# Kernel optimization log

Hardware: AMD Instinct MI355X
Metric: run time of the kernel (lower is better)

The kernel has to match this reference:

```python
import jax, jax.numpy as jnp
import numpy as np

N_CELLS, C_N, K, D_N = 128, 256, 16, 64
G, HS, HM, HMOD, HEADS = 8, 128, 128, 64, 4


def setup_inputs() -> dict:
    key = jax.random.key(0)
    ks = list(jax.random.split(key, 12))
    rng = np.random.default_rng(0)
    # top-K neighbors per neuron within each cell, self excluded, sorted (as in __init__)
    scores = rng.random((N_CELLS, C_N, C_N), dtype=np.float32)
    scores[:, np.arange(C_N), np.arange(C_N)] = -np.inf
    topk = np.argpartition(-scores, K, axis=-1)[..., :K]
    conn_idx = jnp.asarray(np.sort(topk, axis=-1).astype(np.int32))
    cell_to_group = jnp.asarray((np.arange(N_CELLS) % G).astype(np.int32))

    def nrm(k, shape, scale):
        return jax.random.normal(k, shape, dtype=jnp.float32) * scale

    inp = {
        'h': nrm(ks[0], (N_CELLS, C_N, D_N), 1.0),
        'neuron_id': nrm(ks[1], (N_CELLS, C_N, D_N), 0.02),
        'neuron_key': nrm(ks[2], (N_CELLS, C_N, D_N), 0.02),
        'state_w1': nrm(ks[3], (HS, 2 * D_N), (2.0 / (2 * D_N)) ** 0.5),
        'state_b1': jnp.zeros((HS,), jnp.float32),
        'state_gs1': jnp.ones((G, HS), jnp.float32),
        'state_gb1': jnp.zeros((G, HS), jnp.float32),
        'state_w2': nrm(ks[4], (D_N, HS), 0.1 * (2.0 / HS) ** 0.5),
        'state_b2': jnp.zeros((D_N,), jnp.float32),
        'state_gs2': jnp.ones((G, D_N), jnp.float32),
        'state_gb2': jnp.zeros((G, D_N), jnp.float32),
        'msg_w1': nrm(ks[5], (HM, 2 * D_N), (2.0 / (2 * D_N)) ** 0.5),
        'msg_b1': jnp.zeros((HM,), jnp.float32),
        'msg_gs1': jnp.ones((G, HM), jnp.float32),
        'msg_gb1': jnp.zeros((G, HM), jnp.float32),
        'msg_w2': nrm(ks[6], (D_N, HM), 0.1 * (2.0 / HM) ** 0.5),
        'msg_b2': jnp.zeros((D_N,), jnp.float32),
        'msg_gs2': jnp.ones((G, D_N), jnp.float32),
        'msg_gb2': jnp.zeros((G, D_N), jnp.float32),
        'mod_w1': nrm(ks[7], (N_CELLS, D_N, HMOD), (2.0 / D_N) ** 0.5),
        'mod_b1': jnp.zeros((N_CELLS, HMOD), jnp.float32),
        'mod_w2': nrm(ks[8], (N_CELLS, HMOD, D_N), 0.01 * (2.0 / HMOD) ** 0.5),
        'mod_b2': jnp.zeros((N_CELLS, D_N), jnp.float32),
        'conn_idx': conn_idx,
        'cell_to_group': cell_to_group,
    }
    return inp


def reference(h, neuron_id, neuron_key,
              state_w1, state_b1, state_gs1, state_gb1,
              state_w2, state_b2, state_gs2, state_gb2,
              msg_w1, msg_b1, msg_gs1, msg_gb1,
              msg_w2, msg_b2, msg_gs2, msg_gb2,
              mod_w1, mod_b1, mod_w2, mod_b2,
              conn_idx, cell_to_group):
    g = cell_to_group  # [N]
    dh = D_N // HEADS
    gather = jax.vmap(lambda per_cell, idx: per_cell[idx])  # [C,D],[C,K] -> [C,K,D]

    nbr = gather(h, conn_idx)          # [N,C,K,D] neighbor states
    kid = gather(neuron_id, conn_idx)  # [N,C,K,D] neighbor identity vectors

    # multi-head attention weights over the K neighbors
    q = neuron_key.reshape(N_CELLS, C_N, HEADS, dh)
    kk = kid.reshape(N_CELLS, C_N, K, HEADS, dh)
    logits = jnp.einsum('nchd,nckhd->nckh', q, kk) / (dh ** 0.5)
    attn = jax.nn.softmax(logits, axis=2)  # softmax over K

    # per-edge message MLP with per-group gain/bias
    x = jnp.concatenate([nbr, jnp.broadcast_to(h[:, :, None, :], nbr.shape)], axis=-1)  # [N,C,K,2D]
    m1 = jax.nn.gelu(jnp.einsum('nckf,hf->nckh', x, msg_w1) + msg_b1)
    m1 = m1 * msg_gs1[g][:, None, None, :] + msg_gb1[g][:, None, None, :]
    m2 = jnp.einsum('nckh,dh->nckd', m1, msg_w2) + msg_b2
    m2 = m2 * msg_gs2[g][:, None, None, :] + msg_gb2[g][:, None, None, :]

    # attention-weighted aggregation over neighbors
    m2h = m2.reshape(N_CELLS, C_N, K, HEADS, dh)
    agg = jnp.einsum('nckh,nckhd->nchd', attn, m2h).reshape(N_CELLS, C_N, D_N)

    # state-update MLP with per-group gain/bias
    s_in = jnp.concatenate([h, agg], axis=-1)  # [N,C,2D]
    s1 = jax.nn.gelu(jnp.einsum('ncf,hf->nch', s_in, state_w1) + state_b1)
    s1 = s1 * state_gs1[g][:, None, :] + state_gb1[g][:, None, :]
    delta = jnp.einsum('nch,dh->ncd', s1, state_w2) + state_b2
    delta = delta * state_gs2[g][:, None, :] + state_gb2[g][:, None, :]

    # per-cell batched modulation MLP (mod_w1/mod_w2) gating the update
    pooled = h.mean(axis=1)  # [N,D]
    mh = jnp.tanh(jnp.einsum('nd,ndh->nh', pooled, mod_w1) + mod_b1)
    gate = jnp.tanh(jnp.einsum('nh,nho->no', mh, mod_w2) + mod_b2)  # [N,D]

    return h + gate[:, None, :] * delta
```

## Files before the change

kernel.cpp:

```cpp
#include <hip/hip_runtime.h>
#include <hip/hip_bf16.h>

#define N_CELLS 128
#define C_N     256
#define K_NB    16
#define D_N     64
#define G_N     8
#define HS      128
#define HM      128
#define HMOD    64

typedef __bf16 bf16x8 __attribute__((ext_vector_type(8)));
typedef float  f32x4v __attribute__((ext_vector_type(4)));
typedef _Float16 half2_t __attribute__((ext_vector_type(2)));


__device__ __forceinline__ unsigned cvtpk(float lo, float hi) {
    __hip_bfloat162 t = __float22bfloat162_rn(float2{lo, hi});
    return *reinterpret_cast<unsigned*>(&t);
}

__device__ __forceinline__ unsigned short f2bf(float f) {
    return (unsigned short)(cvtpk(f, 0.f) & 0xffffu);
}

__device__ __forceinline__ float bflo(unsigned u) { return __uint_as_float(u << 16); }
__device__ __forceinline__ float bfhi(unsigned u) { return __uint_as_float(u & 0xffff0000u); }

__device__ __forceinline__ half2_t pkrtz(float lo, float hi) {
    return __builtin_bit_cast(half2_t, __builtin_amdgcn_cvt_pkrtz(lo, hi));
}

__device__ __forceinline__ half2_t h2(unsigned u) {
    return __builtin_bit_cast(half2_t, u);
}

__device__ __forceinline__ f32x4v mfma16(uint4 a, uint4 b, f32x4v c) {
    return __builtin_amdgcn_mfma_f32_16x16x32_bf16(
        __builtin_bit_cast(bf16x8, a), __builtin_bit_cast(bf16x8, b), c, 0, 0, 0);
}

__device__ __forceinline__ float gelu_f(float x) {
    float x2 = x * x;
    float u  = x * fmaf(x2, 0.044715f, 1.0f);
    float e  = __expf(1.5957691216057308f * u);
    float r  = __builtin_amdgcn_rcpf(e + 1.0f);
    return x - x * r;
}

__device__ __forceinline__ float sgelu(float x) {
    float e = __expf(-1.702f * x);
    float r = __builtin_amdgcn_rcpf(e + 1.0f);
    return x * r;
}

__device__ __forceinline__ float tanh_fast(float z) {
    float e = __expf(2.0f * z);
    return 1.0f - 2.0f / (e + 1.0f);
}

__device__ __forceinline__ uint4 packf8(const float* p) {
    float4 a = *(const float4*)p, b = *(const float4*)(p + 4);
    return make_uint4(cvtpk(a.x, a.y), cvtpk(a.z, a.w), cvtpk(b.x, b.y), cvtpk(b.z, b.w));
}

__device__ __forceinline__ void load_w2_folded(
    const float* __restrict__ w2, const float* __restrict__ gs1,
    const float* __restrict__ gb1, const float* __restrict__ gs2,
    const float* __restrict__ b2, const float* __restrict__ gb2,
    int g, int lrow, int lgrp, uint4 wf[4][4], float c2[4])
{
    #pragma unroll
    for (int nb2 = 0; nb2 < 4; ++nb2) {
        int d = nb2 * 16 + lrow;
        float gs2d = gs2[g * 64 + d];
        float cgb = 0.0f;
        #pragma unroll
        for (int kf = 0; kf < 4; ++kf) {
            int k0 = kf * 32 + lgrp * 8;
            const float* wp = w2 + d * 128 + k0;
            float4 wa = *(const float4*)wp, wb = *(const float4*)(wp + 4);
            const float* gp = gs1 + g * 128 + k0;
            float4 ga = *(const float4*)gp, gbv = *(const float4*)(gp + 4);
            const float* bp = gb1 + g * 128 + k0;
            float4 ba = *(const float4*)bp, bbv = *(const float4*)(bp + 4);
            cgb += wa.x*ba.x + wa.y*ba.y + wa.z*ba.z + wa.w*ba.w
                 + wb.x*bbv.x + wb.y*bbv.y + wb.z*bbv.z + wb.w*bbv.w;
            wf[nb2][kf] = make_uint4(
                cvtpk(wa.x*ga.x*gs2d,  wa.y*ga.y*gs2d),
                cvtpk(wa.z*ga.z*gs2d,  wa.w*ga.w*gs2d),
                cvtpk(wb.x*gbv.x*gs2d, wb.y*gbv.y*gs2d),
                cvtpk(wb.z*gbv.z*gs2d, wb.w*gbv.w*gs2d));
        }
        cgb += __shfl_xor(cgb, 16);
        cgb += __shfl_xor(cgb, 32);
        c2[nb2] = fmaf(gs2d, cgb + b2[d], gb2[g * 64 + d]);
    }
}


__global__ __launch_bounds__(1024) void gate_kernel(
    const float* __restrict__ h,
    const float* __restrict__ mod_w1, const float* __restrict__ mod_b1,
    const float* __restrict__ mod_w2, const float* __restrict__ mod_b2,
    float* __restrict__ gatep)
{
    __shared__ float red[16][64];
    __shared__ float pooled[64];
    __shared__ float mh[64];
    int n = blockIdx.x, tid = threadIdx.x;
    int d = tid & 63, part = tid >> 6;
    const float* hn = h + (size_t)n * C_N * 64;
    float acc = 0.0f;
    #pragma unroll 4
    for (int i = 0; i < 16; ++i) acc += hn[(part * 16 + i) * 64 + d];
    red[part][d] = acc;
    __syncthreads();
    if (tid < 64) {
        float s = 0.0f;
        #pragma unroll
        for (int p = 0; p < 16; ++p) s += red[p][d];
        pooled[d] = s * (1.0f / 256.0f);
    }
    __syncthreads();
    if (tid < 64) {
        float a1 = mod_b1[n * HMOD + d];
        for (int q = 0; q < 64; ++q)
            a1 = fmaf(pooled[q], mod_w1[((size_t)n * 64 + q) * HMOD + d], a1);
        mh[d] = tanh_fast(a1);
    }
    __syncthreads();
    if (tid < 64) {
        float a2 = mod_b2[n * 64 + d];
        for (int q = 0; q < HMOD; ++q)
            a2 = fmaf(mh[q], mod_w2[((size_t)n * HMOD + q) * 64 + d], a2);
        gatep[n * 64 + d] = tanh_fast(a2);
    }
}


__global__ __launch_bounds__(512, 4) void node_kernel(
    const float* __restrict__ h, const float* __restrict__ msg_w1,
    const float* __restrict__ msg_b1,
    unsigned short* __restrict__ yws, unsigned short* __restrict__ bews)
{
    __shared__ __align__(16) unsigned short ybuf_all[8][16 * 256];
    int tid = threadIdx.x, bid = blockIdx.x;
    int n = bid >> 1;
    int wave = tid >> 6, lane = tid & 63;
    int lrow = lane & 15, lgrp = lane >> 4;
    int c0 = (bid & 1) * 128 + wave * 16;
    unsigned short* ybuf = ybuf_all[wave];

    uint4 bf[2];
    {
        const float* hp = h + ((size_t)n * C_N + (c0 + lrow)) * 64;
        bf[0] = packf8(hp + lgrp * 8);
        bf[1] = packf8(hp + 32 + lgrp * 8);
    }
    for (int nbM = 0; nbM < 16; ++nbM) {
        int o = nbM * 16 + lrow;
        uint4 af[2];
        #pragma unroll
        for (int kf = 0; kf < 2; ++kf) {
            int k = kf * 32 + lgrp * 8;
            const float* wp = (o < 128) ? (msg_w1 + (size_t)o * 128 + k)
                                        : (msg_w1 + (size_t)(o - 128) * 128 + 64 + k);
            af[kf] = packf8(wp);
        }
        f32x4v acc = {0.f, 0.f, 0.f, 0.f};
        acc = mfma16(af[0], bf[0], acc);
        acc = mfma16(af[1], bf[1], acc);
        float4 addv = {0.f, 0.f, 0.f, 0.f};
        if (nbM >= 8) addv = *(const float4*)(msg_b1 + (nbM - 8) * 16 + lgrp * 4);
        uint2 pk = make_uint2(cvtpk(acc[0] + addv.x, acc[1] + addv.y),
                              cvtpk(acc[2] + addv.z, acc[3] + addv.w));
        int byte = lrow * 512 + ((nbM * 32 + lgrp * 8) ^ ((lrow & 7) << 4));
        *reinterpret_cast<uint2*>(reinterpret_cast<char*>(ybuf) + byte) = pk;
    }
    #pragma unroll
    for (int pass = 0; pass < 8; ++pass) {
        int idx = pass * 64 + lane;
        int row = idx >> 5, col = idx & 31;
        int byte = row * 512 + ((col * 16) ^ ((row & 7) << 4));
        uint4 v = *reinterpret_cast<const uint4*>(reinterpret_cast<const char*>(ybuf) + byte);
        size_t rb = (((size_t)n * C_N + c0 + row) * 128) * 2;
        if (col < 16)
            *reinterpret_cast<uint4*>(reinterpret_cast<char*>(yws) + rb + col * 16) = v;
        else
            *reinterpret_cast<uint4*>(reinterpret_cast<char*>(bews) + rb + (col - 16) * 16) = v;
    }
}


__global__ __launch_bounds__(256, 4) void att_kernel(
    const float* __restrict__ neuron_id, const float* __restrict__ neuron_key,
    const int* __restrict__ conn_idx, unsigned* __restrict__ att2)
{
    int tid = threadIdx.x, bid = blockIdx.x;
    int wave = tid >> 6, lane = tid & 63;
    int lrow = lane & 15, t = lane >> 4;
    int base = bid * 64 + wave * 16;

    for (int i = 0; i < 16; ++i) {
        int gidx = base + i;
        int jv = conn_idx[(size_t)gidx * 16 + lrow];
        const float* kp = neuron_id + ((size_t)(gidx & ~255) + jv) * 64 + t * 16;
        const float* qp = neuron_key + (size_t)gidx * 64 + t * 16;
        float4 k0 = *(const float4*)kp,       k1 = *(const float4*)(kp + 4),
               k2 = *(const float4*)(kp + 8), k3 = *(const float4*)(kp + 12);
        float4 q0 = *(const float4*)qp,       q1 = *(const float4*)(qp + 4),
               q2 = *(const float4*)(qp + 8), q3 = *(const float4*)(qp + 12);
        float dt = k0.x*q0.x + k0.y*q0.y + k0.z*q0.z + k0.w*q0.w
                 + k1.x*q1.x + k1.y*q1.y + k1.z*q1.z + k1.w*q1.w
                 + k2.x*q2.x + k2.y*q2.y + k2.z*q2.z + k2.w*q2.w
                 + k3.x*q3.x + k3.y*q3.y + k3.z*q3.z + k3.w*q3.w;
        float lg = dt * 0.25f;
        float mx = lg;
        mx = fmaxf(mx, __shfl_xor(mx, 1));
        mx = fmaxf(mx, __shfl_xor(mx, 2));
        mx = fmaxf(mx, __shfl_xor(mx, 4));
        mx = fmaxf(mx, __shfl_xor(mx, 8));
        float ex = __expf(lg - mx);
        float sm = ex;
        sm += __shfl_xor(sm, 1);
        sm += __shfl_xor(sm, 2);
        sm += __shfl_xor(sm, 4);
        sm += __shfl_xor(sm, 8);
        float av = ex * __builtin_amdgcn_rcpf(sm);
        float avn = __shfl_down(av, 1);
        if ((lrow & 1) == 0) {
            att2[(size_t)gidx * 32 + (lrow >> 1) * 4 + t] =
                __builtin_bit_cast(unsigned, __builtin_amdgcn_cvt_pkrtz(av, avn));
        }
    }
}


__global__ __launch_bounds__(1024, 4) void edge_kernel(
    const unsigned short* __restrict__ yws, const unsigned short* __restrict__ bews,
    const unsigned* __restrict__ att2, const int* __restrict__ conn_idx,
    const float* __restrict__ msg_w2, const float* __restrict__ msg_gs1,
    const float* __restrict__ msg_gb1, const float* __restrict__ msg_gs2,
    const float* __restrict__ msg_b2, const float* __restrict__ msg_gb2,
    const int* __restrict__ cell_to_group,
    unsigned short* __restrict__ aggws)
{
    __shared__ __align__(16) unsigned yl32[C_N * 64];
    __shared__ __align__(16) unsigned attl[128 * 32];
    __shared__ __align__(16) uint4 w2l[16 * 64];
    __shared__ float mb2cl[64];
    __shared__ __align__(16) unsigned short pbuf_all[16][8 * 128];
    __shared__ __align__(16) unsigned short aggT_all[16][2 * 64];
    int tid = threadIdx.x, bid = blockIdx.x;
    int n = bid >> 1;
    int wave = tid >> 6, lane = tid & 63;
    int lrow = lane & 15, lgrp = lane >> 4;
    int base = n * C_N + (bid & 1) * 128 + wave * 8;

    {
        const uint4* src = (const uint4*)((const char*)yws + (size_t)n * C_N * 256);
        uint4* dst = (uint4*)yl32;
        #pragma unroll
        for (int it = 0; it < 4; ++it) dst[it * 1024 + tid] = src[it * 1024 + tid];
        const uint4* asrc = (const uint4*)(att2 + ((size_t)n * 256 + (bid & 1) * 128) * 32);
        ((uint4*)attl)[tid] = asrc[tid];
    }
    if (wave == 0) {
        uint4 w2f[4][4];
        float mb2c[4];
        int g = cell_to_group[n];
        load_w2_folded(msg_w2, msg_gs1, msg_gb1, msg_gs2, msg_b2, msg_gb2,
                       g, lrow, lgrp, w2f, mb2c);
        #pragma unroll
        for (int t = 0; t < 4; ++t) {
            #pragma unroll
            for (int kf = 0; kf < 4; ++kf)
                w2l[(t * 4 + kf) * 64 + lane] = w2f[t][kf];
            if (lgrp == 0) mb2cl[t * 16 + lrow] = mb2c[t];
        }
    }
    __syncthreads();

    float mb2r0 = mb2cl[lrow], mb2r1 = mb2cl[16 + lrow],
          mb2r2 = mb2cl[32 + lrow], mb2r3 = mb2cl[48 + lrow];
    char* pbuf_b = reinterpret_cast<char*>(pbuf_all[wave]);
    char* aggT_b = reinterpret_cast<char*>(aggT_all[wave]);
    const unsigned* bews32 = (const unsigned*)bews;

    #pragma unroll 1
    for (int pr = 0; pr < 4; ++pr) {
        int gA = base + pr * 2, gB = gA + 1;
        int jvA = conn_idx[(size_t)gA * 16 + lrow];
        int jvB = conn_idx[(size_t)gB * 16 + lrow];
        unsigned bepA = bews32[(size_t)gA * 64 + lane];
        unsigned bepB = bews32[(size_t)gB * 64 + lane];
        float beA0 = bflo(bepA), beA1 = bfhi(bepA);
        float beB0 = bflo(bepB), beB1 = bfhi(bepB);
        int laA = wave * 8 + pr * 2, laB = laA + 1;

        float pA[4][2] = {{0.f,0.f},{0.f,0.f},{0.f,0.f},{0.f,0.f}};
        float pB[4][2] = {{0.f,0.f},{0.f,0.f},{0.f,0.f},{0.f,0.f}};

        #pragma unroll
        for (int kp = 0; kp < 8; ++kp) {
            int jA0 = __builtin_amdgcn_readlane(jvA, 2 * kp);
            int jA1 = __builtin_amdgcn_readlane(jvA, 2 * kp + 1);
            int jB0 = __builtin_amdgcn_readlane(jvB, 2 * kp);
            int jB1 = __builtin_amdgcn_readlane(jvB, 2 * kp + 1);
            unsigned uyA0 = yl32[jA0 * 64 + lane];
            unsigned uyA1 = yl32[jA1 * 64 + lane];
            unsigned uyB0 = yl32[jB0 * 64 + lane];
            unsigned uyB1 = yl32[jB1 * 64 + lane];
            uint4 aqA = *reinterpret_cast<const uint4*>(&attl[laA * 32 + kp * 4]);
            uint4 aqB = *reinterpret_cast<const uint4*>(&attl[laB * 32 + kp * 4]);

            float gA00 = sgelu(bflo(uyA0) + beA0), gA01 = sgelu(bfhi(uyA0) + beA1);
            float gA10 = sgelu(bflo(uyA1) + beA0), gA11 = sgelu(bfhi(uyA1) + beA1);
            float gB00 = sgelu(bflo(uyB0) + beB0), gB01 = sgelu(bfhi(uyB0) + beB1);
            float gB10 = sgelu(bflo(uyB1) + beB0), gB11 = sgelu(bfhi(uyB1) + beB1);
            half2_t GA0 = pkrtz(gA00, gA10);
            half2_t GA1 = pkrtz(gA01, gA11);
            half2_t GB0 = pkrtz(gB00, gB10);
            half2_t GB1 = pkrtz(gB01, gB11);

            half2_t hA, hB;
            hA = h2(aqA.x); hB = h2(aqB.x);
            pA[0][0] = __builtin_amdgcn_fdot2(GA0, hA, pA[0][0], false);
            pA[0][1] = __builtin_amdgcn_fdot2(GA1, hA, pA[0][1], false);
            pB[0][0] = __builtin_amdgcn_fdot2(GB0, hB, pB[0][0], false);
            pB[0][1] = __builtin_amdgcn_fdot2(GB1, hB, pB[0][1], false);
            hA = h2(aqA.y); hB = h2(aqB.y);
            pA[1][0] = __builtin_amdgcn_fdot2(GA0, hA, pA[1][0], false);
            pA[1][1] = __builtin_amdgcn_fdot2(GA1, hA, pA[1][1], false);
            pB[1][0] = __builtin_amdgcn_fdot2(GB0, hB, pB[1][0], false);
            pB[1][1] = __builtin_amdgcn_fdot2(GB1, hB, pB[1][1], false);
            hA = h2(aqA.z); hB = h2(aqB.z);
            pA[2][0] = __builtin_amdgcn_fdot2(GA0, hA, pA[2][0], false);
            pA[2][1] = __builtin_amdgcn_fdot2(GA1, hA, pA[2][1], false);
            pB[2][0] = __builtin_amdgcn_fdot2(GB0, hB, pB[2][0], false);
            pB[2][1] = __builtin_amdgcn_fdot2(GB1, hB, pB[2][1], false);
            hA = h2(aqA.w); hB = h2(aqB.w);
            pA[3][0] = __builtin_amdgcn_fdot2(GA0, hA, pA[3][0], false);
            pA[3][1] = __builtin_amdgcn_fdot2(GA1, hA, pA[3][1], false);
            pB[3][0] = __builtin_amdgcn_fdot2(GB0, hB, pB[3][0], false);
            pB[3][1] = __builtin_amdgcn_fdot2(GB1, hB, pB[3][1], false);
        }

        #pragma unroll
        for (int t = 0; t < 4; ++t) {
            int rowA = t * 2, rowB = rowA + 1;
            *reinterpret_cast<unsigned*>(
                pbuf_b + rowA * 256 + ((lane * 4) ^ ((rowA & 7) << 4))) =
                cvtpk(pA[t][0], pA[t][1]);
            *reinterpret_cast<unsigned*>(
                pbuf_b + rowB * 256 + ((lane * 4) ^ ((rowB & 7) << 4))) =
                cvtpk(pB[t][0], pB[t][1]);
        }

        #pragma unroll
        for (int t = 0; t < 4; ++t) {
            f32x4v acc = {0.f, 0.f, 0.f, 0.f};
            #pragma unroll
            for (int kf = 0; kf < 4; ++kf) {
                int row = t * 2 + (lrow & 1);
                uint4 a = *reinterpret_cast<const uint4*>(
                    pbuf_b + row * 256 + ((kf * 64 + lgrp * 16) ^ ((row & 7) << 4)));
                acc = mfma16(a, w2l[(t * 4 + kf) * 64 + lane], acc);
            }
            if (lgrp == 0) {
                float mb = (t == 0) ? mb2r0 : (t == 1) ? mb2r1 : (t == 2) ? mb2r2 : mb2r3;
                #pragma unroll
                for (int r = 0; r < 2; ++r) {
                    float v = acc[r] + mb;
                    int byte = r * 128 + ((((t * 16 + lrow)) * 2) ^ ((r & 7) << 4));
                    *reinterpret_cast<unsigned short*>(aggT_b + byte) = f2bf(v);
                }
            }
        }
        if (lane < 16) {
            int row = lane >> 3, col = lane & 7;
            int byte = row * 128 + ((col * 16) ^ ((row & 7) << 4));
            uint4 v = *reinterpret_cast<const uint4*>(aggT_b + byte);
            *reinterpret_cast<uint4*>(
                (char*)aggws + (size_t)(gA + row) * 128 + col * 16) = v;
        }
    }
}


__global__ __launch_bounds__(512, 4) void state_kernel(
    const float* __restrict__ h, const unsigned short* __restrict__ aggws,
    const float* __restrict__ gatep,
    const float* __restrict__ state_w1, const float* __restrict__ state_b1,
    const float* __restrict__ state_gs1, const float* __restrict__ state_gb1,
    const float* __restrict__ state_w2, const float* __restrict__ state_b2,
    const float* __restrict__ state_gs2, const float* __restrict__ state_gb2,
    const int* __restrict__ cell_to_group, float* __restrict__ out)
{
    __shared__ __align__(16) unsigned short w1s[128 * 128];
    __shared__ __align__(16) unsigned short s1b_all[8][16 * 128];
    int tid = threadIdx.x, bid = blockIdx.x;
    int n = bid >> 1;
    int g = cell_to_group[n];

    for (int idx = tid; idx < 2048; idx += 512) {
        int row = idx >> 4, ch = idx & 15;
        uint4 p = packf8(state_w1 + (size_t)row * 128 + ch * 8);
        int byte = row * 256 + ((ch * 16) ^ ((row & 7) << 4));
        *reinterpret_cast<uint4*>(reinterpret_cast<char*>(w1s) + byte) = p;
    }
    __syncthreads();

    int wave = tid >> 6, lane = tid & 63;
    int lrow = lane & 15, lgrp = lane >> 4;
    int c0 = (bid & 1) * 128 + wave * 16;
    unsigned short* s1b = s1b_all[wave];

    uint4 sB[4];
    {
        const float* hp = h + ((size_t)n * C_N + c0 + lrow) * 64;
        sB[0] = packf8(hp + lgrp * 8);
        sB[1] = packf8(hp + 32 + lgrp * 8);
        const char* ap = (const char*)aggws + ((size_t)n * C_N + c0 + lrow) * 128;
        sB[2] = *reinterpret_cast<const uint4*>(ap + lgrp * 16);
        sB[3] = *reinterpret_cast<const uint4*>(ap + 64 + lgrp * 16);
    }
    for (int nbM = 0; nbM < 8; ++nbM) {
        uint4 wA[4];
        #pragma unroll
        for (int kf = 0; kf < 4; ++kf)
            wA[kf] = *reinterpret_cast<const uint4*>(
                reinterpret_cast<const char*>(w1s) +
                (nbM * 16 + lrow) * 256 + ((kf * 64 + lgrp * 16) ^ ((lrow & 7) << 4)));
        f32x4v acc = {0.f, 0.f, 0.f, 0.f};
        #pragma unroll
        for (int kf = 0; kf < 4; ++kf) acc = mfma16(wA[kf], sB[kf], acc);
        float4 b1q = *(const float4*)(state_b1 + nbM * 16 + lgrp * 4);
        float g0 = gelu_f(acc[0] + b1q.x), g1 = gelu_f(acc[1] + b1q.y);
        float g2 = gelu_f(acc[2] + b1q.z), g3 = gelu_f(acc[3] + b1q.w);
        uint2 pk = make_uint2(cvtpk(g0, g1), cvtpk(g2, g3));
        int byte = lrow * 256 + ((nbM * 32 + lgrp * 8) ^ ((lrow & 7) << 4));
        *reinterpret_cast<uint2*>(reinterpret_cast<char*>(s1b) + byte) = pk;
    }

    uint4 w2sf[4][4];
    float sb2c[4];
    load_w2_folded(state_w2, state_gs1, state_gb1, state_gs2, state_b2, state_gb2,
                   g, lrow, lgrp, w2sf, sb2c);
    uint4 s1A[4];
    #pragma unroll
    for (int kf = 0; kf < 4; ++kf)
        s1A[kf] = *reinterpret_cast<const uint4*>(
            reinterpret_cast<const char*>(s1b) +
            lrow * 256 + ((kf * 64 + lgrp * 16) ^ ((lrow & 7) << 4)));

    float* dT = reinterpret_cast<float*>(s1b);
    #pragma unroll
    for (int nb2 = 0; nb2 < 4; ++nb2) {
        f32x4v acc = {0.f, 0.f, 0.f, 0.f};
        #pragma unroll
        for (int kf = 0; kf < 4; ++kf) acc = mfma16(s1A[kf], w2sf[nb2][kf], acc);
        #pragma unroll
        for (int r = 0; r < 4; ++r) {
            int c = lgrp * 4 + r;
            int d = nb2 * 16 + lrow;
            int byte = c * 256 + ((d * 4) ^ ((c & 7) << 4));
            *reinterpret_cast<float*>(reinterpret_cast<char*>(dT) + byte) = acc[r] + sb2c[nb2];
        }
    }
    #pragma unroll
    for (int pass = 0; pass < 4; ++pass) {
        int idx = pass * 64 + lane;
        int row = idx >> 4, col = idx & 15;
        int byte = row * 256 + ((col * 16) ^ ((row & 7) << 4));
        float4 dv = *reinterpret_cast<const float4*>(reinterpret_cast<const char*>(dT) + byte);
        size_t off = ((size_t)n * C_N + c0 + row) * 64 + col * 4;
        float4 hv = *(const float4*)(h + off);
        float4 gv = *(const float4*)(gatep + n * 64 + col * 4);
        float4 o;
        o.x = fmaf(gv.x, dv.x, hv.x);
        o.y = fmaf(gv.y, dv.y, hv.y);
        o.z = fmaf(gv.z, dv.z, hv.z);
        o.w = fmaf(gv.w, dv.w, hv.w);
        *(float4*)(out + off) = o;
    }
}


extern "C" void kernel_launch(void* const* d_in, const int* in_sizes, int n_in,
                              void* d_out, int out_size, void* d_ws, size_t ws_size,
                              hipStream_t stream) {
    (void)in_sizes; (void)n_in; (void)out_size; (void)ws_size;
    const float* h          = (const float*)d_in[0];
    const float* neuron_id  = (const float*)d_in[1];
    const float* neuron_key = (const float*)d_in[2];
    const float* state_w1   = (const float*)d_in[3];
    const float* state_b1   = (const float*)d_in[4];
    const float* state_gs1  = (const float*)d_in[5];
    const float* state_gb1  = (const float*)d_in[6];
    const float* state_w2   = (const float*)d_in[7];
    const float* state_b2   = (const float*)d_in[8];
    const float* state_gs2  = (const float*)d_in[9];
    const float* state_gb2  = (const float*)d_in[10];
    const float* msg_w1     = (const float*)d_in[11];
    const float* msg_b1     = (const float*)d_in[12];
    const float* msg_gs1    = (const float*)d_in[13];
    const float* msg_gb1    = (const float*)d_in[14];
    const float* msg_w2     = (const float*)d_in[15];
    const float* msg_b2     = (const float*)d_in[16];
    const float* msg_gs2    = (const float*)d_in[17];
    const float* msg_gb2    = (const float*)d_in[18];
    const float* mod_w1     = (const float*)d_in[19];
    const float* mod_b1     = (const float*)d_in[20];
    const float* mod_w2     = (const float*)d_in[21];
    const float* mod_b2     = (const float*)d_in[22];
    const int*   conn_idx   = (const int*)d_in[23];
    const int*   c2g        = (const int*)d_in[24];

    char* ws = (char*)d_ws;
    float*          gatep = (float*)ws;
    unsigned short* yws   = (unsigned short*)(ws + (32u << 10));
    unsigned short* bews  = (unsigned short*)(ws + (32u << 10) + (8u << 20));
    unsigned*       att2  = (unsigned*)(ws + (32u << 10) + (16u << 20));
    unsigned short* aggws = (unsigned short*)(ws + (32u << 10) + (24u << 20));
    float* outp = (float*)d_out;

    gate_kernel<<<dim3(N_CELLS), dim3(1024), 0, stream>>>(
        h, mod_w1, mod_b1, mod_w2, mod_b2, gatep);
    node_kernel<<<dim3(256), dim3(512), 0, stream>>>(
        h, msg_w1, msg_b1, yws, bews);
    att_kernel<<<dim3(512), dim3(256), 0, stream>>>(
        neuron_id, neuron_key, conn_idx, att2);
    edge_kernel<<<dim3(256), dim3(1024), 0, stream>>>(
        yws, bews, att2, conn_idx,
        msg_w2, msg_gs1, msg_gb1, msg_gs2, msg_b2, msg_gb2, c2g, aggws);
    state_kernel<<<dim3(256), dim3(512), 0, stream>>>(
        h, aggws, gatep,
        state_w1, state_b1, state_gs1, state_gb1,
        state_w2, state_b2, state_gs2, state_gb2, c2g, outp);
}
```

Measured before the change: 116.2 us.

## Merge gate, node and attention kernels into one launch; prefetch edge loop loads

The three independent preprocessing kernels (gate MLP, node projection, attention softmax) are merged into a single prep_kernel that dispatches on block index. This removes two launches and lets their work overlap on the GPU. Separately, the edge kernel now software-pipelines its gathers: the next pair's conn_idx/bews values and the next kp step's LDS reads are fetched before the current step is computed. The cost is higher register pressure, and the merged kernel's launch bounds and shared-memory size now apply to all three kinds of block.

```diff
diff --git a/kernel.cpp b/kernel.cpp
--- a/kernel.cpp
+++ b/kernel.cpp
@@ -99,139 +99,131 @@
 }
 
 
-__global__ __launch_bounds__(1024) void gate_kernel(
-    const float* __restrict__ h,
+__global__ __launch_bounds__(512, 2) void prep_kernel(
+    const float* __restrict__ h, const float* __restrict__ neuron_id,
+    const float* __restrict__ neuron_key,
+    const float* __restrict__ msg_w1, const float* __restrict__ msg_b1,
     const float* __restrict__ mod_w1, const float* __restrict__ mod_b1,
     const float* __restrict__ mod_w2, const float* __restrict__ mod_b2,
-    float* __restrict__ gatep)
+    const int* __restrict__ conn_idx,
+    unsigned short* __restrict__ yws, unsigned short* __restrict__ bews,
+    unsigned* __restrict__ att2, float* __restrict__ gatep)
 {
-    __shared__ float red[16][64];
-    __shared__ float pooled[64];
-    __shared__ float mh[64];
-    int n = blockIdx.x, tid = threadIdx.x;
-    int d = tid & 63, part = tid >> 6;
-    const float* hn = h + (size_t)n * C_N * 64;
-    float acc = 0.0f;
-    #pragma unroll 4
-    for (int i = 0; i < 16; ++i) acc += hn[(part * 16 + i) * 64 + d];
-    red[part][d] = acc;
-    __syncthreads();
-    if (tid < 64) {
-        float s = 0.0f;
-        #pragma unroll
-        for (int p = 0; p < 16; ++p) s += red[p][d];
-        pooled[d] = s * (1.0f / 256.0f);
-    }
-    __syncthreads();
-    if (tid < 64) {
-        float a1 = mod_b1[n * HMOD + d];
-        for (int q = 0; q < 64; ++q)
-            a1 = fmaf(pooled[q], mod_w1[((size_t)n * 64 + q) * HMOD + d], a1);
-        mh[d] = tanh_fast(a1);
-    }
-    __syncthreads();
-    if (tid < 64) {
-        float a2 = mod_b2[n * 64 + d];
-        for (int q = 0; q < HMOD; ++q)
-            a2 = fmaf(mh[q], mod_w2[((size_t)n * HMOD + q) * 64 + d], a2);
-        gatep[n * 64 + d] = tanh_fast(a2);
-    }
-}
-
-
-__global__ __launch_bounds__(512, 4) void node_kernel(
-    const float* __restrict__ h, const float* __restrict__ msg_w1,
-    const float* __restrict__ msg_b1,
-    unsigned short* __restrict__ yws, unsigned short* __restrict__ bews)
-{
-    __shared__ __align__(16) unsigned short ybuf_all[8][16 * 256];
+    __shared__ __align__(16) unsigned short shmem[8][16 * 256];
     int tid = threadIdx.x, bid = blockIdx.x;
-    int n = bid >> 1;
     int wave = tid >> 6, lane = tid & 63;
     int lrow = lane & 15, lgrp = lane >> 4;
-    int c0 = (bid & 1) * 128 + wave * 16;
-    unsigned short* ybuf = ybuf_all[wave];
-
-    uint4 bf[2];
-    {
-        const float* hp = h + ((size_t)n * C_N + (c0 + lrow)) * 64;
-        bf[0] = packf8(hp + lgrp * 8);
-        bf[1] = packf8(hp + 32 + lgrp * 8);
-    }
-    for (int nbM = 0; nbM < 16; ++nbM) {
-        int o = nbM * 16 + lrow;
-        uint4 af[2];
-        #pragma unroll
-        for (int kf = 0; kf < 2; ++kf) {
-            int k = kf * 32 + lgrp * 8;
-            const float* wp = (o < 128) ? (msg_w1 + (size_t)o * 128 + k)
-                                        : (msg_w1 + (size_t)(o - 128) * 128 + 64 + k);
-            af[kf] = packf8(wp);
-        }
-        f32x4v acc = {0.f, 0.f, 0.f, 0.f};
-        acc = mfma16(af[0], bf[0], acc);
-        acc = mfma16(af[1], bf[1], acc);
-        float4 addv = {0.f, 0.f, 0.f, 0.f};
-        if (nbM >= 8) addv = *(const float4*)(msg_b1 + (nbM - 8) * 16 + lgrp * 4);
-        uint2 pk = make_uint2(cvtpk(acc[0] + addv.x, acc[1] + addv.y),
-                              cvtpk(acc[2] + addv.z, acc[3] + addv.w));
-        int byte = lrow * 512 + ((nbM * 32 + lgrp * 8) ^ ((lrow & 7) << 4));
-        *reinterpret_cast<uint2*>(reinterpret_cast<char*>(ybuf) + byte) = pk;
-    }
-    #pragma unroll
-    for (int pass = 0; pass < 8; ++pass) {
-        int idx = pass * 64 + lane;
-        int row = idx >> 5, col = idx & 31;
-        int byte = row * 512 + ((col * 16) ^ ((row & 7) << 4));
-        uint4 v = *reinterpret_cast<const uint4*>(reinterpret_cast<const char*>(ybuf) + byte);
-        size_t rb = (((size_t)n * C_N + c0 + row) * 128) * 2;
-        if (col < 16)
-            *reinterpret_cast<uint4*>(reinterpret_cast<char*>(yws) + rb + col * 16) = v;
-        else
-            *reinterpret_cast<uint4*>(reinterpret_cast<char*>(bews) + rb + (col - 16) * 16) = v;
-    }
-}
-
-
-__global__ __launch_bounds__(256, 4) void att_kernel(
-    const float* __restrict__ neuron_id, const float* __restrict__ neuron_key,
-    const int* __restrict__ conn_idx, unsigned* __restrict__ att2)
-{
-    int tid = threadIdx.x, bid = blockIdx.x;
-    int wave = tid >> 6, lane = tid & 63;
-    int lrow = lane & 15, t = lane >> 4;
-    int base = bid * 64 + wave * 16;
-
-    for (int i = 0; i < 16; ++i) {
-        int gidx = base + i;
-        int jv = conn_idx[(size_t)gidx * 16 + lrow];
-        const float* kp = neuron_id + ((size_t)(gidx & ~255) + jv) * 64 + t * 16;
-        const float* qp = neuron_key + (size_t)gidx * 64 + t * 16;
-        float4 k0 = *(const float4*)kp,       k1 = *(const float4*)(kp + 4),
-               k2 = *(const float4*)(kp + 8), k3 = *(const float4*)(kp + 12);
-        float4 q0 = *(const float4*)qp,       q1 = *(const float4*)(qp + 4),
-               q2 = *(const float4*)(qp + 8), q3 = *(const float4*)(qp + 12);
-        float dt = k0.x*q0.x + k0.y*q0.y + k0.z*q0.z + k0.w*q0.w
-                 + k1.x*q1.x + k1.y*q1.y + k1.z*q1.z + k1.w*q1.w
-                 + k2.x*q2.x + k2.y*q2.y + k2.z*q2.z + k2.w*q2.w
-                 + k3.x*q3.x + k3.y*q3.y + k3.z*q3.z + k3.w*q3.w;
-        float lg = dt * 0.25f;
-        float mx = lg;
-        mx = fmaxf(mx, __shfl_xor(mx, 1));
-        mx = fmaxf(mx, __shfl_xor(mx, 2));
-        mx = fmaxf(mx, __shfl_xor(mx, 4));
-        mx = fmaxf(mx, __shfl_xor(mx, 8));
-        float ex = __expf(lg - mx);
-        float sm = ex;
-        sm += __shfl_xor(sm, 1);
-        sm += __shfl_xor(sm, 2);
-        sm += __shfl_xor(sm, 4);
-        sm += __shfl_xor(sm, 8);
-        float av = ex * __builtin_amdgcn_rcpf(sm);
-        float avn = __shfl_down(av, 1);
-        if ((lrow & 1) == 0) {
-            att2[(size_t)gidx * 32 + (lrow >> 1) * 4 + t] =
-                __builtin_bit_cast(unsigned, __builtin_amdgcn_cvt_pkrtz(av, avn));
+
+    if (bid < 256) {
+        int n = bid >> 1;
+        int c0 = (bid & 1) * 128 + wave * 16;
+        unsigned short* ybuf = shmem[wave];
+
+        uint4 bf[2];
+        {
+            const float* hp = h + ((size_t)n * C_N + (c0 + lrow)) * 64;
+            bf[0] = packf8(hp + lgrp * 8);
+            bf[1] = packf8(hp + 32 + lgrp * 8);
+        }
+        for (int nbM = 0; nbM < 16; ++nbM) {
+            int o = nbM * 16 + lrow;
+            uint4 af[2];
+            #pragma unroll
+            for (int kf = 0; kf < 2; ++kf) {
+                int k = kf * 32 + lgrp * 8;
+                const float* wp = (o < 128) ? (msg_w1 + (size_t)o * 128 + k)
+                                            : (msg_w1 + (size_t)(o - 128) * 128 + 64 + k);
+                af[kf] = packf8(wp);
+            }
+            f32x4v acc = {0.f, 0.f, 0.f, 0.f};
+            acc = mfma16(af[0], bf[0], acc);
+            acc = mfma16(af[1], bf[1], acc);
+            float4 addv = {0.f, 0.f, 0.f, 0.f};
+            if (nbM >= 8) addv = *(const float4*)(msg_b1 + (nbM - 8) * 16 + lgrp * 4);
+            uint2 pk = make_uint2(cvtpk(acc[0] + addv.x, acc[1] + addv.y),
+                                  cvtpk(acc[2] + addv.z, acc[3] + addv.w));
+            int byte = lrow * 512 + ((nbM * 32 + lgrp * 8) ^ ((lrow & 7) << 4));
+            *reinterpret_cast<uint2*>(reinterpret_cast<char*>(ybuf) + byte) = pk;
+        }
+        #pragma unroll
+        for (int pass = 0; pass < 8; ++pass) {
+            int idx = pass * 64 + lane;
+            int row = idx >> 5, col = idx & 31;
+            int byte = row * 512 + ((col * 16) ^ ((row & 7) << 4));
+            uint4 v = *reinterpret_cast<const uint4*>(
+                reinterpret_cast<const char*>(ybuf) + byte);
+            size_t rb = (((size_t)n * C_N + c0 + row) * 128) * 2;
+            if (col < 16)
+                *reinterpret_cast<uint4*>(reinterpret_cast<char*>(yws) + rb + col * 16) = v;
+            else
+                *reinterpret_cast<uint4*>(reinterpret_cast<char*>(bews) + rb + (col - 16) * 16) = v;
+        }
+    } else if (bid < 512) {
+        int t = lgrp;
+        int base = (bid - 256) * 128 + wave * 16;
+        for (int i = 0; i < 16; ++i) {
+            int gidx = base + i;
+            int jv = conn_idx[(size_t)gidx * 16 + lrow];
+            const float* kp = neuron_id + ((size_t)(gidx & ~255) + jv) * 64 + t * 16;
+            const float* qp = neuron_key + (size_t)gidx * 64 + t * 16;
+            float4 k0 = *(const float4*)kp,       k1 = *(const float4*)(kp + 4),
+                   k2 = *(const float4*)(kp + 8), k3 = *(const float4*)(kp + 12);
+            float4 q0 = *(const float4*)qp,       q1 = *(const float4*)(qp + 4),
+                   q2 = *(const float4*)(qp + 8), q3 = *(const float4*)(qp + 12);
+            float dt = k0.x*q0.x + k0.y*q0.y + k0.z*q0.z + k0.w*q0.w
+                     + k1.x*q1.x + k1.y*q1.y + k1.z*q1.z + k1.w*q1.w
+                     + k2.x*q2.x + k2.y*q2.y + k2.z*q2.z + k2.w*q2.w
+                     + k3.x*q3.x + k3.y*q3.y + k3.z*q3.z + k3.w*q3.w;
+            float lg = dt * 0.25f;
+            float mx = lg;
+            mx = fmaxf(mx, __shfl_xor(mx, 1));
+            mx = fmaxf(mx, __shfl_xor(mx, 2));
+            mx = fmaxf(mx, __shfl_xor(mx, 4));
+            mx = fmaxf(mx, __shfl_xor(mx, 8));
+            float ex = __expf(lg - mx);
+            float sm = ex;
+            sm += __shfl_xor(sm, 1);
+            sm += __shfl_xor(sm, 2);
+            sm += __shfl_xor(sm, 4);
+            sm += __shfl_xor(sm, 8);
+            float av = ex * __builtin_amdgcn_rcpf(sm);
+            float avn = __shfl_down(av, 1);
+            if ((lrow & 1) == 0) {
+                att2[(size_t)gidx * 32 + (lrow >> 1) * 4 + t] =
+                    __builtin_bit_cast(unsigned, __builtin_amdgcn_cvt_pkrtz(av, avn));
+            }
+        }
+    } else {
+        int n = bid - 512;
+        float* red   = reinterpret_cast<float*>(shmem);
+        float* pooled = red + 8 * 64;
+        float* mh     = pooled + 64;
+        int d = lane, part = wave;
+        const float* hn = h + (size_t)n * C_N * 64;
+        float acc = 0.0f;
+        #pragma unroll 4
+        for (int i = 0; i < 32; ++i) acc += hn[(part * 32 + i) * 64 + d];
+        red[part * 64 + d] = acc;
+        __syncthreads();
+        if (tid < 64) {
+            float s = 0.0f;
+            #pragma unroll
+            for (int p = 0; p < 8; ++p) s += red[p * 64 + d];
+            pooled[d] = s * (1.0f / 256.0f);
+        }
+        __syncthreads();
+        if (tid < 64) {
+            float a1 = mod_b1[n * HMOD + d];
+            for (int q = 0; q < 64; ++q)
+                a1 = fmaf(pooled[q], mod_w1[((size_t)n * 64 + q) * HMOD + d], a1);
+            mh[d] = tanh_fast(a1);
+        }
+        __syncthreads();
+        if (tid < 64) {
+            float a2 = mod_b2[n * 64 + d];
+            for (int q = 0; q < HMOD; ++q)
+                a2 = fmaf(mh[q], mod_w2[((size_t)n * HMOD + q) * 64 + d], a2);
+            gatep[n * 64 + d] = tanh_fast(a2);
         }
     }
 }
@@ -288,13 +280,21 @@
     char* aggT_b = reinterpret_cast<char*>(aggT_all[wave]);
     const unsigned* bews32 = (const unsigned*)bews;
 
+    int jvA = conn_idx[(size_t)base * 16 + lrow];
+    int jvB = conn_idx[(size_t)(base + 1) * 16 + lrow];
+    unsigned bepA = bews32[(size_t)base * 64 + lane];
+    unsigned bepB = bews32[(size_t)(base + 1) * 64 + lane];
+
     #pragma unroll 1
     for (int pr = 0; pr < 4; ++pr) {
-        int gA = base + pr * 2, gB = gA + 1;
-        int jvA = conn_idx[(size_t)gA * 16 + lrow];
-        int jvB = conn_idx[(size_t)gB * 16 + lrow];
-        unsigned bepA = bews32[(size_t)gA * 64 + lane];
-        unsigned bepB = bews32[(size_t)gB * 64 + lane];
+        int gA = base + pr * 2;
+        int prn = (pr < 3) ? (pr + 1) : 3;
+        int gAn = base + prn * 2;
+        int jvA_n = conn_idx[(size_t)gAn * 16 + lrow];
+        int jvB_n = conn_idx[(size_t)(gAn + 1) * 16 + lrow];
+        unsigned bepA_n = bews32[(size_t)gAn * 64 + lane];
+        unsigned bepB_n = bews32[(size_t)(gAn + 1) * 64 + lane];
+
         float beA0 = bflo(bepA), beA1 = bfhi(bepA);
         float beB0 = bflo(bepB), beB1 = bfhi(bepB);
         int laA = wave * 8 + pr * 2, laB = laA + 1;
@@ -302,49 +302,73 @@
         float pA[4][2] = {{0.f,0.f},{0.f,0.f},{0.f,0.f},{0.f,0.f}};
         float pB[4][2] = {{0.f,0.f},{0.f,0.f},{0.f,0.f},{0.f,0.f}};
 
+        unsigned uyA0c, uyA1c, uyB0c, uyB1c;
+        uint4 aqAc, aqBc;
+        {
+            int jA0 = __builtin_amdgcn_readlane(jvA, 0);
+            int jA1 = __builtin_amdgcn_readlane(jvA, 1);
+            int jB0 = __builtin_amdgcn_readlane(jvB, 0);
+            int jB1 = __builtin_amdgcn_readlane(jvB, 1);
+            uyA0c = yl32[jA0 * 64 + lane];
+            uyA1c = yl32[jA1 * 64 + lane];
+            uyB0c = yl32[jB0 * 64 + lane];
+            uyB1c = yl32[jB1 * 64 + lane];
+            aqAc = *reinterpret_cast<const uint4*>(&attl[laA * 32]);
+            aqBc = *reinterpret_cast<const uint4*>(&attl[laB * 32]);
+        }
+
         #pragma unroll
         for (int kp = 0; kp < 8; ++kp) {
-            int jA0 = __builtin_amdgcn_readlane(jvA, 2 * kp);
-            int jA1 = __builtin_amdgcn_readlane(jvA, 2 * kp + 1);
-            int jB0 = __builtin_amdgcn_readlane(jvB, 2 * kp);
-            int jB1 = __builtin_amdgcn_readlane(jvB, 2 * kp + 1);
-            unsigned uyA0 = yl32[jA0 * 64 + lane];
-            unsigned uyA1 = yl32[jA1 * 64 + lane];
-            unsigned uyB0 = yl32[jB0 * 64 + lane];
-            unsigned uyB1 = yl32[jB1 * 64 + lane];
-            uint4 aqA = *reinterpret_cast<const uint4*>(&attl[laA * 32 + kp * 4]);
-            uint4 aqB = *reinterpret_cast<const uint4*>(&attl[laB * 32 + kp * 4]);
-
-            float gA00 = sgelu(bflo(uyA0) + beA0), gA01 = sgelu(bfhi(uyA0) + beA1);
-            float gA10 = sgelu(bflo(uyA1) + beA0), gA11 = sgelu(bfhi(uyA1) + beA1);
-            float gB00 = sgelu(bflo(uyB0) + beB0), gB01 = sgelu(bfhi(uyB0) + beB1);
-            float gB10 = sgelu(bflo(uyB1) + beB0), gB11 = sgelu(bfhi(uyB1) + beB1);
+            unsigned uyA0n, uyA1n, uyB0n, uyB1n;
+            uint4 aqAn2, aqBn2;
+            if (kp < 7) {
+                int jA0 = __builtin_amdgcn_readlane(jvA, 2 * kp + 2);
+                int jA1 = __builtin_amdgcn_readlane(jvA, 2 * kp + 3);
+                int jB0 = __builtin_amdgcn_readlane(jvB, 2 * kp + 2);
+                int jB1 = __builtin_amdgcn_readlane(jvB, 2 * kp + 3);
+                uyA0n = yl32[jA0 * 64 + lane];
+                uyA1n = yl32[jA1 * 64 + lane];
+                uyB0n = yl32[jB0 * 64 + lane];
+                uyB1n = yl32[jB1 * 64 + lane];
+                aqAn2 = *reinterpret_cast<const uint4*>(&attl[laA * 32 + (kp + 1) * 4]);
+                aqBn2 = *reinterpret_cast<const uint4*>(&attl[laB * 32 + (kp + 1) * 4]);
+            }
+
+            float gA00 = sgelu(bflo(uyA0c) + beA0), gA01 = sgelu(bfhi(uyA0c) + beA1);
+            float gA10 = sgelu(bflo(uyA1c) + beA0), gA11 = sgelu(bfhi(uyA1c) + beA1);
+            float gB00 = sgelu(bflo(uyB0c) + beB0), gB01 = sgelu(bfhi(uyB0c) + beB1);
+            float gB10 = sgelu(bflo(uyB1c) + beB0), gB11 = sgelu(bfhi(uyB1c) + beB1);
             half2_t GA0 = pkrtz(gA00, gA10);
             half2_t GA1 = pkrtz(gA01, gA11);
             half2_t GB0 = pkrtz(gB00, gB10);
             half2_t GB1 = pkrtz(gB01, gB11);
 
             half2_t hA, hB;
-            hA = h2(aqA.x); hB = h2(aqB.x);
+            hA = h2(aqAc.x); hB = h2(aqBc.x);
             pA[0][0] = __builtin_amdgcn_fdot2(GA0, hA, pA[0][0], false);
             pA[0][1] = __builtin_amdgcn_fdot2(GA1, hA, pA[0][1], false);
             pB[0][0] = __builtin_amdgcn_fdot2(GB0, hB, pB[0][0], false);
             pB[0][1] = __builtin_amdgcn_fdot2(GB1, hB, pB[0][1], false);
-            hA = h2(aqA.y); hB = h2(aqB.y);
+            hA = h2(aqAc.y); hB = h2(aqBc.y);
             pA[1][0] = __builtin_amdgcn_fdot2(GA0, hA, pA[1][0], false);
             pA[1][1] = __builtin_amdgcn_fdot2(GA1, hA, pA[1][1], false);
             pB[1][0] = __builtin_amdgcn_fdot2(GB0, hB, pB[1][0], false);
             pB[1][1] = __builtin_amdgcn_fdot2(GB1, hB, pB[1][1], false);
-            hA = h2(aqA.z); hB = h2(aqB.z);
+            hA = h2(aqAc.z); hB = h2(aqBc.z);
             pA[2][0] = __builtin_amdgcn_fdot2(GA0, hA, pA[2][0], false);
             pA[2][1] = __builtin_amdgcn_fdot2(GA1, hA, pA[2][1], false);
             pB[2][0] = __builtin_amdgcn_fdot2(GB0, hB, pB[2][0], false);
             pB[2][1] = __builtin_amdgcn_fdot2(GB1, hB, pB[2][1], false);
-            hA = h2(aqA.w); hB = h2(aqB.w);
+            hA = h2(aqAc.w); hB = h2(aqBc.w);
             pA[3][0] = __builtin_amdgcn_fdot2(GA0, hA, pA[3][0], false);
             pA[3][1] = __builtin_amdgcn_fdot2(GA1, hA, pA[3][1], false);
             pB[3][0] = __builtin_amdgcn_fdot2(GB0, hB, pB[3][0], false);
             pB[3][1] = __builtin_amdgcn_fdot2(GB1, hB, pB[3][1], false);
+
+            if (kp < 7) {
+                uyA0c = uyA0n; uyA1c = uyA1n; uyB0c = uyB0n; uyB1c = uyB1n;
+                aqAc = aqAn2; aqBc = aqBn2;
+            }
         }
 
         #pragma unroll
@@ -385,6 +409,7 @@
             *reinterpret_cast<uint4*>(
                 (char*)aggws + (size_t)(gA + row) * 128 + col * 16) = v;
         }
+        jvA = jvA_n; jvB = jvB_n; bepA = bepA_n; bepB = bepB_n;
     }
 }
 
@@ -526,12 +551,10 @@
     unsigned short* aggws = (unsigned short*)(ws + (32u << 10) + (24u << 20));
     float* outp = (float*)d_out;
 
-    gate_kernel<<<dim3(N_CELLS), dim3(1024), 0, stream>>>(
-        h, mod_w1, mod_b1, mod_w2, mod_b2, gatep);
-    node_kernel<<<dim3(256), dim3(512), 0, stream>>>(
-        h, msg_w1, msg_b1, yws, bews);
-    att_kernel<<<dim3(512), dim3(256), 0, stream>>>(
-        neuron_id, neuron_key, conn_idx, att2);
+    prep_kernel<<<dim3(640), dim3(512), 0, stream>>>(
+        h, neuron_id, neuron_key, msg_w1, msg_b1,
+        mod_w1, mod_b1, mod_w2, mod_b2, conn_idx,
+        yws, bews, att2, gatep);
     edge_kernel<<<dim3(256), dim3(1024), 0, stream>>>(
         yws, bews, att2, conn_idx,
         msg_w2, msg_gs1, msg_gb1, msg_gs2, msg_b2, msg_gb2, c2g, aggws);
```

Result: faster. 112.1 us (-3.6%).

## Merge gate, node and attention kernels into one block-specialized prep kernel

Applied to the files above, without the earlier changes.

Three independent preprocessing kernels (node projection, attention softmax, gate MLP) are combined into a single launch where block ranges dispatch to each role. This removes two kernel launches and their inter-kernel gaps and lets the independent work run concurrently across CUs. The edge kernel's launch bounds are also changed to an explicit waves-per-EU attribute. The merged kernel uses 512-thread blocks with a shared LDS footprint sized for the largest role, which may lower occupancy for the attention and gate blocks.

```diff
diff --git a/kernel.cpp b/kernel.cpp
--- a/kernel.cpp
+++ b/kernel.cpp
@@ -99,145 +99,139 @@
 }
 
 
-__global__ __launch_bounds__(1024) void gate_kernel(
-    const float* __restrict__ h,
+__global__ __launch_bounds__(512, 2) void prep_kernel(
+    const float* __restrict__ h, const float* __restrict__ neuron_id,
+    const float* __restrict__ neuron_key,
+    const float* __restrict__ msg_w1, const float* __restrict__ msg_b1,
     const float* __restrict__ mod_w1, const float* __restrict__ mod_b1,
     const float* __restrict__ mod_w2, const float* __restrict__ mod_b2,
-    float* __restrict__ gatep)
+    const int* __restrict__ conn_idx,
+    unsigned short* __restrict__ yws, unsigned short* __restrict__ bews,
+    unsigned* __restrict__ att2, float* __restrict__ gatep)
 {
-    __shared__ float red[16][64];
-    __shared__ float pooled[64];
-    __shared__ float mh[64];
-    int n = blockIdx.x, tid = threadIdx.x;
-    int d = tid & 63, part = tid >> 6;
-    const float* hn = h + (size_t)n * C_N * 64;
-    float acc = 0.0f;
-    #pragma unroll 4
-    for (int i = 0; i < 16; ++i) acc += hn[(part * 16 + i) * 64 + d];
-    red[part][d] = acc;
-    __syncthreads();
-    if (tid < 64) {
-        float s = 0.0f;
-        #pragma unroll
-        for (int p = 0; p < 16; ++p) s += red[p][d];
-        pooled[d] = s * (1.0f / 256.0f);
-    }
-    __syncthreads();
-    if (tid < 64) {
-        float a1 = mod_b1[n * HMOD + d];
-        for (int q = 0; q < 64; ++q)
-            a1 = fmaf(pooled[q], mod_w1[((size_t)n * 64 + q) * HMOD + d], a1);
-        mh[d] = tanh_fast(a1);
-    }
-    __syncthreads();
-    if (tid < 64) {
-        float a2 = mod_b2[n * 64 + d];
-        for (int q = 0; q < HMOD; ++q)
-            a2 = fmaf(mh[q], mod_w2[((size_t)n * HMOD + q) * 64 + d], a2);
-        gatep[n * 64 + d] = tanh_fast(a2);
-    }
-}
-
-
-__global__ __launch_bounds__(512, 4) void node_kernel(
-    const float* __restrict__ h, const float* __restrict__ msg_w1,
-    const float* __restrict__ msg_b1,
-    unsigned short* __restrict__ yws, unsigned short* __restrict__ bews)
-{
-    __shared__ __align__(16) unsigned short ybuf_all[8][16 * 256];
+    __shared__ __align__(16) unsigned short shmem[8][16 * 256];
     int tid = threadIdx.x, bid = blockIdx.x;
-    int n = bid >> 1;
     int wave = tid >> 6, lane = tid & 63;
     int lrow = lane & 15, lgrp = lane >> 4;
-    int c0 = (bid & 1) * 128 + wave * 16;
-    unsigned short* ybuf = ybuf_all[wave];
-
-    uint4 bf[2];
-    {
-        const float* hp = h + ((size_t)n * C_N + (c0 + lrow)) * 64;
-        bf[0] = packf8(hp + lgrp * 8);
-        bf[1] = packf8(hp + 32 + lgrp * 8);
-    }
-    for (int nbM = 0; nbM < 16; ++nbM) {
-        int o = nbM * 16 + lrow;
-        uint4 af[2];
-        #pragma unroll
-        for (int kf = 0; kf < 2; ++kf) {
-            int k = kf * 32 + lgrp * 8;
-            const float* wp = (o < 128) ? (msg_w1 + (size_t)o * 128 + k)
-                                        : (msg_w1 + (size_t)(o - 128) * 128 + 64 + k);
-            af[kf] = packf8(wp);
-        }
-        f32x4v acc = {0.f, 0.f, 0.f, 0.f};
-        acc = mfma16(af[0], bf[0], acc);
-        acc = mfma16(af[1], bf[1], acc);
-        float4 addv = {0.f, 0.f, 0.f, 0.f};
-        if (nbM >= 8) addv = *(const float4*)(msg_b1 + (nbM - 8) * 16 + lgrp * 4);
-        uint2 pk = make_uint2(cvtpk(acc[0] + addv.x, acc[1] + addv.y),
-                              cvtpk(acc[2] + addv.z, acc[3] + addv.w));
-        int byte = lrow * 512 + ((nbM * 32 + lgrp * 8) ^ ((lrow & 7) << 4));
-        *reinterpret_cast<uint2*>(reinterpret_cast<char*>(ybuf) + byte) = pk;
-    }
-    #pragma unroll
-    for (int pass = 0; pass < 8; ++pass) {
-        int idx = pass * 64 + lane;
-        int row = idx >> 5, col = idx & 31;
-        int byte = row * 512 + ((col * 16) ^ ((row & 7) << 4));
-        uint4 v = *reinterpret_cast<const uint4*>(reinterpret_cast<const char*>(ybuf) + byte);
-        size_t rb = (((size_t)n * C_N + c0 + row) * 128) * 2;
-        if (col < 16)
-            *reinterpret_cast<uint4*>(reinterpret_cast<char*>(yws) + rb + col * 16) = v;
-        else
-            *reinterpret_cast<uint4*>(reinterpret_cast<char*>(bews) + rb + (col - 16) * 16) = v;
-    }
-}
-
-
-__global__ __launch_bounds__(256, 4) void att_kernel(
-    const float* __restrict__ neuron_id, const float* __restrict__ neuron_key,
-    const int* __restrict__ conn_idx, unsigned* __restrict__ att2)
-{
-    int tid = threadIdx.x, bid = blockIdx.x;
-    int wave = tid >> 6, lane = tid & 63;
-    int lrow = lane & 15, t = lane >> 4;
-    int base = bid * 64 + wave * 16;
-
-    for (int i = 0; i < 16; ++i) {
-        int gidx = base + i;
-        int jv = conn_idx[(size_t)gidx * 16 + lrow];
-        const float* kp = neuron_id + ((size_t)(gidx & ~255) + jv) * 64 + t * 16;
-        const float* qp = neuron_key + (size_t)gidx * 64 + t * 16;
-        float4 k0 = *(const float4*)kp,       k1 = *(const float4*)(kp + 4),
-               k2 = *(const float4*)(kp + 8), k3 = *(const float4*)(kp + 12);
-        float4 q0 = *(const float4*)qp,       q1 = *(const float4*)(qp + 4),
-               q2 = *(const float4*)(qp + 8), q3 = *(const float4*)(qp + 12);
-        float dt = k0.x*q0.x + k0.y*q0.y + k0.z*q0.z + k0.w*q0.w
-                 + k1.x*q1.x + k1.y*q1.y + k1.z*q1.z + k1.w*q1.w
-                 + k2.x*q2.x + k2.y*q2.y + k2.z*q2.z + k2.w*q2.w
-                 + k3.x*q3.x + k3.y*q3.y + k3.z*q3.z + k3.w*q3.w;
-        float lg = dt * 0.25f;
-        float mx = lg;
-        mx = fmaxf(mx, __shfl_xor(mx, 1));
-        mx = fmaxf(mx, __shfl_xor(mx, 2));
-        mx = fmaxf(mx, __shfl_xor(mx, 4));
-        mx = fmaxf(mx, __shfl_xor(mx, 8));
-        float ex = __expf(lg - mx);
-        float sm = ex;
-        sm += __shfl_xor(sm, 1);
-        sm += __shfl_xor(sm, 2);
-        sm += __shfl_xor(sm, 4);
-        sm += __shfl_xor(sm, 8);
-        float av = ex * __builtin_amdgcn_rcpf(sm);
-        float avn = __shfl_down(av, 1);
-        if ((lrow & 1) == 0) {
-            att2[(size_t)gidx * 32 + (lrow >> 1) * 4 + t] =
-                __builtin_bit_cast(unsigned, __builtin_amdgcn_cvt_pkrtz(av, avn));
-        }
-    }
-}
-
-
-__global__ __launch_bounds__(1024, 4) void edge_kernel(
+
+    if (bid < 256) {
+        int n = bid >> 1;
+        int c0 = (bid & 1) * 128 + wave * 16;
+        unsigned short* ybuf = shmem[wave];
+
+        uint4 bf[2];
+        {
+            const float* hp = h + ((size_t)n * C_N + (c0 + lrow)) * 64;
+            bf[0] = packf8(hp + lgrp * 8);
+            bf[1] = packf8(hp + 32 + lgrp * 8);
+        }
+        for (int nbM = 0; nbM < 16; ++nbM) {
+            int o = nbM * 16 + lrow;
+            uint4 af[2];
+            #pragma unroll
+            for (int kf = 0; kf < 2; ++kf) {
+                int k = kf * 32 + lgrp * 8;
+                const float* wp = (o < 128) ? (msg_w1 + (size_t)o * 128 + k)
+                                            : (msg_w1 + (size_t)(o - 128) * 128 + 64 + k);
+                af[kf] = packf8(wp);
+            }
+            f32x4v acc = {0.f, 0.f, 0.f, 0.f};
+            acc = mfma16(af[0], bf[0], acc);
+            acc = mfma16(af[1], bf[1], acc);
+            float4 addv = {0.f, 0.f, 0.f, 0.f};
+            if (nbM >= 8) addv = *(const float4*)(msg_b1 + (nbM - 8) * 16 + lgrp * 4);
+            uint2 pk = make_uint2(cvtpk(acc[0] + addv.x, acc[1] + addv.y),
+                                  cvtpk(acc[2] + addv.z, acc[3] + addv.w));
+            int byte = lrow * 512 + ((nbM * 32 + lgrp * 8) ^ ((lrow & 7) << 4));
+            *reinterpret_cast<uint2*>(reinterpret_cast<char*>(ybuf) + byte) = pk;
+        }
+        #pragma unroll
+        for (int pass = 0; pass < 8; ++pass) {
+            int idx = pass * 64 + lane;
+            int row = idx >> 5, col = idx & 31;
+            int byte = row * 512 + ((col * 16) ^ ((row & 7) << 4));
+            uint4 v = *reinterpret_cast<const uint4*>(
+                reinterpret_cast<const char*>(ybuf) + byte);
+            size_t rb = (((size_t)n * C_N + c0 + row) * 128) * 2;
+            if (col < 16)
+                *reinterpret_cast<uint4*>(reinterpret_cast<char*>(yws) + rb + col * 16) = v;
+            else
+                *reinterpret_cast<uint4*>(reinterpret_cast<char*>(bews) + rb + (col - 16) * 16) = v;
+        }
+    } else if (bid < 512) {
+        int t = lgrp;
+        int base = (bid - 256) * 128 + wave * 16;
+        for (int i = 0; i < 16; ++i) {
+            int gidx = base + i;
+            int jv = conn_idx[(size_t)gidx * 16 + lrow];
+            const float* kp = neuron_id + ((size_t)(gidx & ~255) + jv) * 64 + t * 16;
+            const float* qp = neuron_key + (size_t)gidx * 64 + t * 16;
+            float4 k0 = *(const float4*)kp,       k1 = *(const float4*)(kp + 4),
+                   k2 = *(const float4*)(kp + 8), k3 = *(const float4*)(kp + 12);
+            float4 q0 = *(const float4*)qp,       q1 = *(const float4*)(qp + 4),
+                   q2 = *(const float4*)(qp + 8), q3 = *(const float4*)(qp + 12);
+            float dt = k0.x*q0.x + k0.y*q0.y + k0.z*q0.z + k0.w*q0.w
+                     + k1.x*q1.x + k1.y*q1.y + k1.z*q1.z + k1.w*q1.w
+                     + k2.x*q2.x + k2.y*q2.y + k2.z*q2.z + k2.w*q2.w
+                     + k3.x*q3.x + k3.y*q3.y + k3.z*q3.z + k3.w*q3.w;
+            float lg = dt * 0.25f;
+            float mx = lg;
+            mx = fmaxf(mx, __shfl_xor(mx, 1));
+            mx = fmaxf(mx, __shfl_xor(mx, 2));
+            mx = fmaxf(mx, __shfl_xor(mx, 4));
+            mx = fmaxf(mx, __shfl_xor(mx, 8));
+            float ex = __expf(lg - mx);
+            float sm = ex;
+            sm += __shfl_xor(sm, 1);
+            sm += __shfl_xor(sm, 2);
+            sm += __shfl_xor(sm, 4);
+            sm += __shfl_xor(sm, 8);
+            float av = ex * __builtin_amdgcn_rcpf(sm);
+            float avn = __shfl_down(av, 1);
+            if ((lrow & 1) == 0) {
+                att2[(size_t)gidx * 32 + (lrow >> 1) * 4 + t] =
+                    __builtin_bit_cast(unsigned, __builtin_amdgcn_cvt_pkrtz(av, avn));
+            }
+        }
+    } else {
+        int n = bid - 512;
+        float* red   = reinterpret_cast<float*>(shmem);
+        float* pooled = red + 8 * 64;
+        float* mh     = pooled + 64;
+        int d = lane, part = wave;
+        const float* hn = h + (size_t)n * C_N * 64;
+        float acc = 0.0f;
+        #pragma unroll 4
+        for (int i = 0; i < 32; ++i) acc += hn[(part * 32 + i) * 64 + d];
+        red[part * 64 + d] = acc;
+        __syncthreads();
+        if (tid < 64) {
+            float s = 0.0f;
+            #pragma unroll
+            for (int p = 0; p < 8; ++p) s += red[p * 64 + d];
+            pooled[d] = s * (1.0f / 256.0f);
+        }
+        __syncthreads();
+        if (tid < 64) {
+            float a1 = mod_b1[n * HMOD + d];
+            for (int q = 0; q < 64; ++q)
+                a1 = fmaf(pooled[q], mod_w1[((size_t)n * 64 + q) * HMOD + d], a1);
+            mh[d] = tanh_fast(a1);
+        }
+        __syncthreads();
+        if (tid < 64) {
+            float a2 = mod_b2[n * 64 + d];
+            for (int q = 0; q < HMOD; ++q)
+                a2 = fmaf(mh[q], mod_w2[((size_t)n * HMOD + q) * 64 + d], a2);
+            gatep[n * 64 + d] = tanh_fast(a2);
+        }
+    }
+}
+
+
+__global__ __launch_bounds__(1024)
+__attribute__((amdgpu_waves_per_eu(4, 4)))
+void edge_kernel(
     const unsigned short* __restrict__ yws, const unsigned short* __restrict__ bews,
     const unsigned* __restrict__ att2, const int* __restrict__ conn_idx,
     const float* __restrict__ msg_w2, const float* __restrict__ msg_gs1,
@@ -526,12 +520,10 @@
     unsigned short* aggws = (unsigned short*)(ws + (32u << 10) + (24u << 20));
     float* outp = (float*)d_out;
 
-    gate_kernel<<<dim3(N_CELLS), dim3(1024), 0, stream>>>(
-        h, mod_w1, mod_b1, mod_w2, mod_b2, gatep);
-    node_kernel<<<dim3(256), dim3(512), 0, stream>>>(
-        h, msg_w1, msg_b1, yws, bews);
-    att_kernel<<<dim3(512), dim3(256), 0, stream>>>(
-        neuron_id, neuron_key, conn_idx, att2);
+    prep_kernel<<<dim3(640), dim3(512), 0, stream>>>(
+        h, neuron_id, neuron_key, msg_w1, msg_b1,
+        mod_w1, mod_b1, mod_w2, mod_b2, conn_idx,
+        yws, bews, att2, gatep);
     edge_kernel<<<dim3(256), dim3(1024), 0, stream>>>(
         yws, bews, att2, conn_idx,
         msg_w2, msg_gs1, msg_gb1, msg_gs2, msg_b2, msg_gb2, c2g, aggws);
```

After: 105.2 us. 9.4% less time.
